# Kernel tuning notes

Hardware: AMD Instinct MI355X
Metric: run time of the kernel (lower is better)

## Reference

```python
import jax, jax.numpy as jnp
import numpy as np

D_MODEL = 256
N_HEADS = 8
HEAD_DIM = D_MODEL // N_HEADS


def setup_inputs() -> dict:
    key = jax.random.key(0)
    k1, k2, k3, k4, k5, k6, k7 = jax.random.split(key, 7)
    B, T, N, D = 4, 32, 32, D_MODEL
    x = jax.random.normal(k1, (B, T, N, D), dtype=jnp.float32)
    bias_features = jax.random.normal(k2, (B, T, N, N, D), dtype=jnp.float32)
    # alive mask, mostly True so rows are rarely fully masked
    mask = jax.random.uniform(k3, (B, T, N)) < 0.9
    s = 1.0 / np.sqrt(D)
    w_qkv = jax.random.normal(k4, (D, 3 * D), dtype=jnp.float32) * s
    b_qkv = jnp.zeros((3 * D,), dtype=jnp.float32)
    w_proj = jax.random.normal(k5, (D, D), dtype=jnp.float32) * s
    b_proj = jnp.zeros((D,), dtype=jnp.float32)
    return {"x": x, "bias_features": bias_features, "mask": mask,
            "w_qkv": w_qkv, "b_qkv": b_qkv, "w_proj": w_proj, "b_proj": b_proj}


def reference(x, bias_features, mask, w_qkv, b_qkv, w_proj, b_proj):
    B, T, N, D = x.shape
    H, Dh = N_HEADS, D // N_HEADS
    Bt = B * T
    xf = x.reshape(Bt, N, D)
    qkv = xf @ w_qkv + b_qkv                       # (Bt, N, 3D)
    q, k, v = jnp.split(qkv, 3, axis=-1)
    q = q.reshape(Bt, N, H, Dh)
    k = k.reshape(Bt, N, H, Dh)
    v = v.reshape(Bt, N, H, Dh)
    b_geo = bias_features.reshape(Bt, N, N, H, Dh)
    k_pair = k[:, None] + b_geo                    # (Bt, N, N, H, Dh)
    v_pair = v[:, None] + b_geo
    # scores: (Bt, H, N, N)
    scores = jnp.einsum('bihd,bijhd->bhij', q, k_pair) * (Dh ** -0.5)
    mask_flat = mask.reshape(Bt, 1, 1, N)
    scores = jnp.where(mask_flat, scores, -jnp.inf)
    max_scores = jnp.max(scores, axis=-1, keepdims=True)
    is_nan_row = max_scores == -jnp.inf
    scores_safe = jnp.where(is_nan_row, 0.0, scores)
    attn = jax.nn.softmax(scores_safe, axis=-1)
    attn = jnp.where(is_nan_row, 0.0, attn)
    out = jnp.einsum('bhij,bijhd->bihd', attn, v_pair).reshape(Bt, N, D)
    out = out.reshape(B, T, N, D)
    return out @ w_proj + b_proj
```

## Files before the change

kernel.cpp:

```cpp
#include <hip/hip_runtime.h>
#include <math.h>

typedef __attribute__((ext_vector_type(8))) short bf16x8;
typedef __attribute__((ext_vector_type(4))) short bf16x4;
typedef __attribute__((ext_vector_type(4))) float f32x4;

__device__ inline ushort f2bf(float f) {
    union { float f; uint u; } v; v.f = f;
    uint u = v.u;
    return (ushort)((u + 0x7fff + ((u >> 16) & 1)) >> 16);
}
__device__ inline float bf2f(ushort u) {
    union { uint u; float f; } v; v.u = ((uint)u) << 16; return v.f;
}

typedef __attribute__((address_space(1))) const void global_void;
typedef __attribute__((address_space(3))) void lds_void;
__device__ inline void gl_lds16(const void* g, void* l) {
    __builtin_amdgcn_global_load_lds((global_void*)g, (lds_void*)l, 16, 0, 0);
}

template<int BM, int BN, int WGM, int WGN, int MODE>
__global__ __launch_bounds__(WGM * WGN * 64) void gemm_fused(
    const void* __restrict__ Ap, const float* __restrict__ Bw, int ldb,
    const float* __restrict__ bias,
    void* __restrict__ C0, void* __restrict__ C1, void* __restrict__ C2,
    int K, int N)
{
    constexpr int BK = 32;
    constexpr int NT = WGM * WGN * 64;
    constexpr int WM = BM / (WGM * 16);
    constexpr int WN = BN / (WGN * 16);

    __shared__ ushort As[BM * BK];
    __shared__ ushort Bs[BN * BK];

    const int tid = threadIdx.x;
    const int lane = tid & 63, wid = tid >> 6;
    const int wm = wid / WGN, wn = wid % WGN;
    const int row0 = blockIdx.y * BM, col0 = blockIdx.x * BN;
    const int frow = lane & 15, fg = lane >> 4;

    f32x4 acc[WM][WN] = {};

    for (int k0 = 0; k0 < K; k0 += BK) {
        if constexpr (MODE == 0) {
            #pragma unroll
            for (int ci = tid; ci < BM * 8; ci += NT) {
                int r = ci >> 3, kq = ci & 7, g = kq >> 1;
                float4 v = *(const float4*)((const float*)Ap + (size_t)(row0 + r) * K + k0 + kq * 4);
                bf16x4 o;
                o[0] = (short)f2bf(v.x); o[1] = (short)f2bf(v.y);
                o[2] = (short)f2bf(v.z); o[3] = (short)f2bf(v.w);
                *(bf16x4*)&As[r * 32 + ((g ^ ((r >> 1) & 3)) << 3) + (kq & 1) * 4] = o;
            }
        } else {
            #pragma unroll
            for (int ci = tid; ci < BM * 4; ci += NT) {
                int r = ci >> 2, g = ci & 3;
                bf16x8 v = *(const bf16x8*)((const ushort*)Ap + (size_t)(row0 + r) * K + k0 + g * 8);
                *(bf16x8*)&As[r * 32 + ((g ^ ((r >> 1) & 3)) << 3)] = v;
            }
        }
        #pragma unroll
        for (int ci = tid; ci < BN * 8; ci += NT) {
            int kk = ci & 31, n4 = ci >> 5;
            float4 v = *(const float4*)&Bw[(size_t)(k0 + kk) * ldb + col0 + n4 * 4];
            float vv[4] = {v.x, v.y, v.z, v.w};
            #pragma unroll
            for (int e = 0; e < 4; ++e) {
                int n = n4 * 4 + e;
                Bs[n * 32 + (((kk >> 3) ^ ((n >> 1) & 3)) << 3) + (kk & 7)] = f2bf(vv[e]);
            }
        }
        __syncthreads();

        bf16x8 af[WM], bfr[WN];
        #pragma unroll
        for (int m = 0; m < WM; ++m) {
            int r = (wm * WM + m) * 16 + frow;
            af[m] = *(const bf16x8*)&As[r * 32 + ((fg ^ ((r >> 1) & 3)) << 3)];
        }
        #pragma unroll
        for (int n = 0; n < WN; ++n) {
            int r = (wn * WN + n) * 16 + frow;
            bfr[n] = *(const bf16x8*)&Bs[r * 32 + ((fg ^ ((r >> 1) & 3)) << 3)];
        }
        #pragma unroll
        for (int m = 0; m < WM; ++m)
            #pragma unroll
            for (int n = 0; n < WN; ++n)
                acc[m][n] = __builtin_amdgcn_mfma_f32_16x16x32_bf16(
                    af[m], bfr[n], acc[m][n], 0, 0, 0);
        __syncthreads();
    }

    #pragma unroll
    for (int n = 0; n < WN; ++n) {
        int gcol = col0 + (wn * WN + n) * 16 + frow;
        float bv = bias[gcol];
        if constexpr (MODE == 0) {
            int b = gcol >> 8, c = gcol & 255;
            ushort* dst = (b == 0) ? (ushort*)C0 : (b == 1) ? (ushort*)C1 : (ushort*)C2;
            #pragma unroll
            for (int m = 0; m < WM; ++m) {
                int grow0 = row0 + (wm * WM + m) * 16 + fg * 4;
                #pragma unroll
                for (int r = 0; r < 4; ++r)
                    dst[(size_t)(grow0 + r) * 256 + c] = f2bf(acc[m][n][r] + bv);
            }
        } else {
            float* dst = (float*)C0;
            #pragma unroll
            for (int m = 0; m < WM; ++m) {
                int grow0 = row0 + (wm * WM + m) * 16 + fg * 4;
                #pragma unroll
                for (int r = 0; r < 4; ++r)
                    dst[(size_t)(grow0 + r) * N + gcol] = acc[m][n][r] + bv;
            }
        }
    }
}

__global__ __launch_bounds__(256, 2) void relattn_kernel(
    const ushort* __restrict__ qb, const ushort* __restrict__ kb,
    const ushort* __restrict__ vb, const float* __restrict__ bias,
    const int* __restrict__ mask, ushort* __restrict__ attn_out)
{
    __shared__ float slab[2][8192];

    const int b = blockIdx.x;
    const int item0 = b << 3;
    const int bt = b >> 2;
    const int tid = threadIdx.x;
    const int w = tid >> 6, L = tid & 63;
    const int hw = L >> 5;
    const int h = 2 * w + hw;
    const int jd = L & 31;

    const bool alive = (mask[bt * 32 + jd] != 0);

    bf16x8 k8[4];
    const ushort* krow = kb + (size_t)(bt * 32 + jd) * 256 + h * 32;
    #pragma unroll
    for (int t = 0; t < 4; ++t) k8[t] = *(const bf16x8*)(krow + t * 8);

    ushort vreg[32];
    const ushort* vbase = vb + (size_t)bt * 8192 + tid;
    #pragma unroll
    for (int jj = 0; jj < 32; ++jj) vreg[jj] = vbase[(size_t)jj * 256];

    bf16x8 qreg[2][4];
    #pragma unroll
    for (int t = 0; t < 4; ++t)
        qreg[0][t] = *(const bf16x8*)(qb + (size_t)item0 * 256 + h * 32 + t * 8);

    const float* bbase = bias + (size_t)item0 * 8192;

    auto stage = [&](int item_idx, int buf) {
        const float* bi = bbase + (size_t)item_idx * 8192;
        #pragma unroll
        for (int g = 0; g < 8; ++g) {
            int j = g * 4 + w;
            gl_lds16(bi + j * 256 + ((L ^ (j & 7)) << 2), &slab[buf][j * 256]);
        }
    };

    stage(0, 0);
    __syncthreads();

    #pragma unroll
    for (int it = 0; it < 8; ++it) {
        const float* cur = slab[it & 1];
        const int qcur = it & 1 ? 1 : 0;

        if (it < 7) {
            #pragma unroll
            for (int t = 0; t < 4; ++t)
                qreg[(it + 1) & 1][t] = *(const bf16x8*)(
                    qb + (size_t)(item0 + it + 1) * 256 + h * 32 + t * 8);
            stage(it + 1, (it + 1) & 1);
        }

        float s = 0.f;
        #pragma unroll
        for (int t = 0; t < 4; ++t) {
            bf16x8 q8 = qreg[qcur][t];
            int m0 = h * 8 + 2 * t;
            f32x4 b0 = *(const f32x4*)&cur[jd * 256 + ((m0 ^ (jd & 7)) << 2)];
            f32x4 b1 = *(const f32x4*)&cur[jd * 256 + (((m0 + 1) ^ (jd & 7)) << 2)];
            s += bf2f((ushort)q8[0]) * (bf2f((ushort)k8[t][0]) + b0[0])
               + bf2f((ushort)q8[1]) * (bf2f((ushort)k8[t][1]) + b0[1])
               + bf2f((ushort)q8[2]) * (bf2f((ushort)k8[t][2]) + b0[2])
               + bf2f((ushort)q8[3]) * (bf2f((ushort)k8[t][3]) + b0[3])
               + bf2f((ushort)q8[4]) * (bf2f((ushort)k8[t][4]) + b1[0])
               + bf2f((ushort)q8[5]) * (bf2f((ushort)k8[t][5]) + b1[1])
               + bf2f((ushort)q8[6]) * (bf2f((ushort)k8[t][6]) + b1[2])
               + bf2f((ushort)q8[7]) * (bf2f((ushort)k8[t][7]) + b1[3]);
        }
        s *= 0.17677669529663687f;
        s = alive ? s : -__builtin_inff();

        float m = s;
        #pragma unroll
        for (int off = 16; off; off >>= 1) m = fmaxf(m, __shfl_xor(m, off));
        const bool dead = (m == -__builtin_inff());
        float p = alive ? __expf(s - m) : 0.f;
        float l = p;
        #pragma unroll
        for (int off = 16; off; off >>= 1) l += __shfl_xor(l, off);
        float pn = dead ? 0.f : p / l;

        const int half32 = L & 32;
        const int cc = tid >> 2, clo = tid & 3;
        float o0 = 0.f, o1 = 0.f, o2 = 0.f, o3 = 0.f;
        #pragma unroll
        for (int jq = 0; jq < 8; ++jq) {
            int j0 = jq * 4;
            float pa = __shfl(pn, half32 | (j0 + 0));
            float pb = __shfl(pn, half32 | (j0 + 1));
            float pc = __shfl(pn, half32 | (j0 + 2));
            float pd = __shfl(pn, half32 | (j0 + 3));
            float ba = cur[(j0 + 0) * 256 + ((((cc & 63) ^ ((j0 + 0) & 7)) << 2) | clo)];
            float bb = cur[(j0 + 1) * 256 + ((((cc & 63) ^ ((j0 + 1) & 7)) << 2) | clo)];
            float bc = cur[(j0 + 2) * 256 + ((((cc & 63) ^ ((j0 + 2) & 7)) << 2) | clo)];
            float bd = cur[(j0 + 3) * 256 + ((((cc & 63) ^ ((j0 + 3) & 7)) << 2) | clo)];
            o0 += pa * (bf2f(vreg[j0 + 0]) + ba);
            o1 += pb * (bf2f(vreg[j0 + 1]) + bb);
            o2 += pc * (bf2f(vreg[j0 + 2]) + bc);
            o3 += pd * (bf2f(vreg[j0 + 3]) + bd);
        }
        attn_out[(size_t)(item0 + it) * 256 + tid] = f2bf((o0 + o1) + (o2 + o3));

        if (it < 7) __syncthreads();
    }
}

extern "C" void kernel_launch(void* const* d_in, const int* in_sizes, int n_in,
                              void* d_out, int out_size, void* d_ws, size_t ws_size,
                              hipStream_t stream) {
    const float* x      = (const float*)d_in[0];
    const float* bias_f = (const float*)d_in[1];
    const int*   mask   = (const int*)d_in[2];
    const float* w_qkv  = (const float*)d_in[3];
    const float* b_qkv  = (const float*)d_in[4];
    const float* w_proj = (const float*)d_in[5];
    const float* b_proj = (const float*)d_in[6];
    float* out = (float*)d_out;

    ushort* qb = (ushort*)d_ws;
    ushort* kb = qb + (size_t)4096 * 256;
    ushort* vb = kb + (size_t)4096 * 256;
    ushort* ao = vb + (size_t)4096 * 256;

    gemm_fused<64, 64, 2, 2, 0><<<dim3(12, 64), 256, 0, stream>>>(
        x, w_qkv, 768, b_qkv, qb, kb, vb, 256, 768);

    relattn_kernel<<<512, 256, 0, stream>>>(qb, kb, vb, bias_f, mask, ao);

    gemm_fused<32, 64, 1, 4, 1><<<dim3(4, 128), 256, 0, stream>>>(
        ao, w_proj, 256, b_proj, out, nullptr, nullptr, 256, 256);
}
```

Before: 55.95 us.

## Use column-per-thread layout with register-held bias and shuffle-reduced scores

```diff
diff --git a/kernel.cpp b/kernel.cpp
--- a/kernel.cpp
+++ b/kernel.cpp
@@ -134,71 +134,64 @@
     const int bt = b >> 2;
     const int tid = threadIdx.x;
     const int w = tid >> 6, L = tid & 63;
-    const int hw = L >> 5;
-    const int h = 2 * w + hw;
+    const int col = w * 64 + L;
     const int jd = L & 31;
+    const int half32 = L & 32;
 
     const bool alive = (mask[bt * 32 + jd] != 0);
 
-    bf16x8 k8[4];
-    const ushort* krow = kb + (size_t)(bt * 32 + jd) * 256 + h * 32;
-    #pragma unroll
-    for (int t = 0; t < 4; ++t) k8[t] = *(const bf16x8*)(krow + t * 8);
-
-    ushort vreg[32];
-    const ushort* vbase = vb + (size_t)bt * 8192 + tid;
-    #pragma unroll
-    for (int jj = 0; jj < 32; ++jj) vreg[jj] = vbase[(size_t)jj * 256];
-
-    bf16x8 qreg[2][4];
-    #pragma unroll
-    for (int t = 0; t < 4; ++t)
-        qreg[0][t] = *(const bf16x8*)(qb + (size_t)item0 * 256 + h * 32 + t * 8);
+    ushort kreg[32], vreg[32];
+    #pragma unroll
+    for (int j = 0; j < 32; ++j) {
+        kreg[j] = kb[(size_t)(bt * 32 + j) * 256 + col];
+        vreg[j] = vb[(size_t)(bt * 32 + j) * 256 + col];
+    }
+    ushort qreg[8];
+    #pragma unroll
+    for (int it = 0; it < 8; ++it)
+        qreg[it] = qb[(size_t)(item0 + it) * 256 + col];
 
     const float* bbase = bias + (size_t)item0 * 8192;
 
-    auto stage = [&](int item_idx, int buf) {
-        const float* bi = bbase + (size_t)item_idx * 8192;
-        #pragma unroll
-        for (int g = 0; g < 8; ++g) {
-            int j = g * 4 + w;
-            gl_lds16(bi + j * 256 + ((L ^ (j & 7)) << 2), &slab[buf][j * 256]);
+    auto stage = [&](int idx, int buf) {
+        const float* bi = bbase + (size_t)idx * 8192;
+        #pragma unroll
+        for (int jj = 0; jj < 8; ++jj) {
+            int j = w * 8 + jj;
+            gl_lds16(bi + j * 256 + L * 4, &slab[buf][j * 256]);
         }
     };
 
     stage(0, 0);
-    __syncthreads();
-
+
+    float oprev = 0.f;
     #pragma unroll
     for (int it = 0; it < 8; ++it) {
+        __syncthreads();
+
+        if (it > 0)
+            attn_out[(size_t)(item0 + it - 1) * 256 + tid] = f2bf(oprev);
+        if (it < 7) stage(it + 1, (it + 1) & 1);
+
         const float* cur = slab[it & 1];
-        const int qcur = it & 1 ? 1 : 0;
-
-        if (it < 7) {
-            #pragma unroll
-            for (int t = 0; t < 4; ++t)
-                qreg[(it + 1) & 1][t] = *(const bf16x8*)(
-                    qb + (size_t)(item0 + it + 1) * 256 + h * 32 + t * 8);
-            stage(it + 1, (it + 1) & 1);
-        }
-
-        float s = 0.f;
-        #pragma unroll
-        for (int t = 0; t < 4; ++t) {
-            bf16x8 q8 = qreg[qcur][t];
-            int m0 = h * 8 + 2 * t;
-            f32x4 b0 = *(const f32x4*)&cur[jd * 256 + ((m0 ^ (jd & 7)) << 2)];
-            f32x4 b1 = *(const f32x4*)&cur[jd * 256 + (((m0 + 1) ^ (jd & 7)) << 2)];
-            s += bf2f((ushort)q8[0]) * (bf2f((ushort)k8[t][0]) + b0[0])
-               + bf2f((ushort)q8[1]) * (bf2f((ushort)k8[t][1]) + b0[1])
-               + bf2f((ushort)q8[2]) * (bf2f((ushort)k8[t][2]) + b0[2])
-               + bf2f((ushort)q8[3]) * (bf2f((ushort)k8[t][3]) + b0[3])
-               + bf2f((ushort)q8[4]) * (bf2f((ushort)k8[t][4]) + b1[0])
-               + bf2f((ushort)q8[5]) * (bf2f((ushort)k8[t][5]) + b1[1])
-               + bf2f((ushort)q8[6]) * (bf2f((ushort)k8[t][6]) + b1[2])
-               + bf2f((ushort)q8[7]) * (bf2f((ushort)k8[t][7]) + b1[3]);
-        }
-        s *= 0.17677669529663687f;
+
+        float breg[32];
+        #pragma unroll
+        for (int j = 0; j < 32; ++j) breg[j] = cur[j * 256 + col];
+
+        const float qf = bf2f(qreg[it]);
+        float sreg = 0.f;
+        #pragma unroll
+        for (int j = 0; j < 32; ++j) {
+            float part = qf * (bf2f(kreg[j]) + breg[j]);
+            part += __shfl_xor(part, 1);
+            part += __shfl_xor(part, 2);
+            part += __shfl_xor(part, 4);
+            part += __shfl_xor(part, 8);
+            part += __shfl_xor(part, 16);
+            if (j == jd) sreg = part;
+        }
+        float s = sreg * 0.17677669529663687f;
         s = alive ? s : -__builtin_inff();
 
         float m = s;
@@ -211,8 +204,6 @@
         for (int off = 16; off; off >>= 1) l += __shfl_xor(l, off);
         float pn = dead ? 0.f : p / l;
 
-        const int half32 = L & 32;
-        const int cc = tid >> 2, clo = tid & 3;
         float o0 = 0.f, o1 = 0.f, o2 = 0.f, o3 = 0.f;
         #pragma unroll
         for (int jq = 0; jq < 8; ++jq) {
@@ -221,19 +212,14 @@
             float pb = __shfl(pn, half32 | (j0 + 1));
             float pc = __shfl(pn, half32 | (j0 + 2));
             float pd = __shfl(pn, half32 | (j0 + 3));
-            float ba = cur[(j0 + 0) * 256 + ((((cc & 63) ^ ((j0 + 0) & 7)) << 2) | clo)];
-            float bb = cur[(j0 + 1) * 256 + ((((cc & 63) ^ ((j0 + 1) & 7)) << 2) | clo)];
-            float bc = cur[(j0 + 2) * 256 + ((((cc & 63) ^ ((j0 + 2) & 7)) << 2) | clo)];
-            float bd = cur[(j0 + 3) * 256 + ((((cc & 63) ^ ((j0 + 3) & 7)) << 2) | clo)];
-            o0 += pa * (bf2f(vreg[j0 + 0]) + ba);
-            o1 += pb * (bf2f(vreg[j0 + 1]) + bb);
-            o2 += pc * (bf2f(vreg[j0 + 2]) + bc);
-            o3 += pd * (bf2f(vreg[j0 + 3]) + bd);
-        }
-        attn_out[(size_t)(item0 + it) * 256 + tid] = f2bf((o0 + o1) + (o2 + o3));
-
-        if (it < 7) __syncthreads();
-    }
+            o0 += pa * (bf2f(vreg[j0 + 0]) + breg[j0 + 0]);
+            o1 += pb * (bf2f(vreg[j0 + 1]) + breg[j0 + 1]);
+            o2 += pc * (bf2f(vreg[j0 + 2]) + breg[j0 + 2]);
+            o3 += pd * (bf2f(vreg[j0 + 3]) + breg[j0 + 3]);
+        }
+        oprev = (o0 + o1) + (o2 + o3);
+    }
+    attn_out[(size_t)(item0 + 7) * 256 + tid] = f2bf(oprev);
 }
 
 extern "C" void kernel_launch(void* const* d_in, const int* in_sizes, int n_in,
```

Result: slower. 93.37 us (+66.9%).
